# Kernel tuning notes

Hardware: AMD Instinct MI355X
Metric: run time of the kernel (lower is better)

## Reference

```python
import jax, jax.numpy as jnp
import numpy as np

N_NODES = 50000
N_EDGES = 500000
IN_DIM = 256
HID = 128
OUT_DIM = 7
N_LAYERS = 3
N_PAIRS = 100000
BATCH = 65536
BN_EPS = 1e-5


def setup_inputs() -> dict:
    key = jax.random.key(0)
    ks = jax.random.split(key, 24)
    s = 0.05
    inp = {
        "feat": jax.random.normal(ks[0], (N_NODES, IN_DIM), dtype=jnp.float32),
        "src": jax.random.randint(ks[1], (N_EDGES,), 0, N_NODES),
        "dst": jax.random.randint(ks[2], (N_EDGES,), 0, N_NODES),
        "ppi_pairs": jax.random.randint(ks[3], (N_PAIRS, 2), 0, N_NODES),
        "idx": jax.random.randint(ks[4], (BATCH,), 0, N_PAIRS),
        # GINConv 0 (input layer): 2-layer MLP IN_DIM->HID->HID
        "eps": jnp.zeros((N_LAYERS,), jnp.float32),
        "w1_in": jax.random.normal(ks[5], (IN_DIM, HID)) * s,
        "b1_in": jnp.zeros((HID,), jnp.float32),
        "w2_in": jax.random.normal(ks[6], (HID, HID)) * s,
        "b2_in": jnp.zeros((HID,), jnp.float32),
        # GINConv 1..2 (hidden layers), stacked
        "hw1": jax.random.normal(ks[7], (N_LAYERS - 1, HID, HID)) * s,
        "hb1": jnp.zeros((N_LAYERS - 1, HID), jnp.float32),
        "hw2": jax.random.normal(ks[8], (N_LAYERS - 1, HID, HID)) * s,
        "hb2": jnp.zeros((N_LAYERS - 1, HID), jnp.float32),
        # BatchNorm (eval mode) params per layer, stacked
        "bn_gamma": jnp.ones((N_LAYERS, HID), jnp.float32),
        "bn_beta": jnp.zeros((N_LAYERS, HID), jnp.float32),
        "bn_mean": jax.random.normal(ks[9], (N_LAYERS, HID)) * 0.1,
        "bn_var": jax.random.uniform(ks[10], (N_LAYERS, HID), minval=0.5, maxval=1.5),
        # final node linear
        "lin_w": jax.random.normal(ks[11], (HID, HID)) * s,
        "lin_b": jnp.zeros((HID,), jnp.float32),
        # interaction MLP: 2*HID -> HID -> OUT_DIM
        "int_w1": jax.random.normal(ks[12], (2 * HID, HID)) * s,
        "int_b1": jnp.zeros((HID,), jnp.float32),
        "int_w2": jax.random.normal(ks[13], (HID, OUT_DIM)) * s,
        "int_b2": jnp.zeros((OUT_DIM,), jnp.float32),
    }
    return inp


def _gin_layer(h, src, dst, eps_i, w1, b1, w2, b2, gamma, beta, mean, var):
    # sum-aggregate neighbor features: scatter-add messages src -> dst
    agg = jax.ops.segment_sum(h[src], dst, num_segments=N_NODES)
    h = (1.0 + eps_i) * h + agg
    # 2-layer MLP with ReLU after each linear (as in nn.Sequential)
    h = jax.nn.relu(h @ w1 + b1)
    h = jax.nn.relu(h @ w2 + b2)
    # BatchNorm1d, eval mode (running stats)
    h = (h - mean) * jax.lax.rsqrt(var + BN_EPS) * gamma + beta
    # trailing ReLU (dropout is identity at eval)
    return jax.nn.relu(h)


def reference(feat, src, dst, ppi_pairs, idx, eps, w1_in, b1_in, w2_in, b2_in,
              hw1, hb1, hw2, hb2, bn_gamma, bn_beta, bn_mean, bn_var,
              lin_w, lin_b, int_w1, int_b1, int_w2, int_b2):
    h = _gin_layer(feat, src, dst, eps[0], w1_in, b1_in, w2_in, b2_in,
                   bn_gamma[0], bn_beta[0], bn_mean[0], bn_var[0])
    for i in range(N_LAYERS - 1):
        h = _gin_layer(h, src, dst, eps[i + 1], hw1[i], hb1[i], hw2[i], hb2[i],
                       bn_gamma[i + 1], bn_beta[i + 1], bn_mean[i + 1], bn_var[i + 1])
    h = jax.nn.relu(h @ lin_w + lin_b)  # final node projection (dropout = identity)
    pairs = ppi_pairs[idx]              # [B, 2] node-id pairs
    h1 = h[pairs[:, 0]]
    h2 = h[pairs[:, 1]]
    z = jnp.concatenate([h1, h2], axis=1)        # [B, 2*HID]
    z = jax.nn.relu(z @ int_w1 + int_b1)         # (dropout = identity)
    return z @ int_w2 + int_b2                   # [B, OUT_DIM]
```

## Files before the change

kernel.cpp:

```cpp
#include <hip/hip_runtime.h>

#define N_NODES 50000
#define N_EDGES 500000
#define IN_DIM  256
#define HID     128
#define OUT_DIM 7
#define NPAIRS  100000
#define BATCH   65536
#define BN_EPS  1e-5f

#define SCAN_BLK 196

typedef __attribute__((ext_vector_type(8))) short bf16x8;
typedef __attribute__((ext_vector_type(4))) float f32x4;

__device__ inline float b2f(ushort u) {
  unsigned int x = ((unsigned int)u) << 16;
  return __uint_as_float(x);
}
__device__ inline ushort f2b(float f) {
  unsigned int x = __float_as_uint(f);
  unsigned int r = (x + 0x7fffu + ((x >> 16) & 1u)) >> 16;
  return (ushort)r;
}

__global__ void hist_kernel(const int* __restrict__ dst, int* __restrict__ deg) {
  int e = blockIdx.x * blockDim.x + threadIdx.x;
  if (e < N_EDGES) atomicAdd(&deg[dst[e]], 1);
}

__global__ __launch_bounds__(256) void scan_partial(const int* __restrict__ deg,
                                                    int* __restrict__ part) {
  __shared__ int s[256];
  int t = threadIdx.x;
  int i = blockIdx.x * 256 + t;
  s[t] = (i < N_NODES) ? deg[i] : 0;
  __syncthreads();
  for (int off = 128; off > 0; off >>= 1) {
    if (t < off) s[t] += s[t + off];
    __syncthreads();
  }
  if (t == 0) part[blockIdx.x] = s[0];
}

__global__ __launch_bounds__(256) void scan_offsets(int* __restrict__ part) {
  __shared__ int s[256];
  int t = threadIdx.x;
  int v = (t < SCAN_BLK) ? part[t] : 0;
  s[t] = v;
  __syncthreads();
  for (int off = 1; off < 256; off <<= 1) {
    int u = (t >= off) ? s[t - off] : 0;
    __syncthreads();
    s[t] += u;
    __syncthreads();
  }
  if (t < SCAN_BLK) part[t] = s[t] - v;
}

__global__ __launch_bounds__(256) void scan_final(const int* __restrict__ deg,
                                                  const int* __restrict__ part,
                                                  int* __restrict__ row_ptr,
                                                  int* __restrict__ cursor) {
  __shared__ int s[256];
  int t = threadIdx.x;
  int i = blockIdx.x * 256 + t;
  int v = (i < N_NODES) ? deg[i] : 0;
  s[t] = v;
  __syncthreads();
  for (int off = 1; off < 256; off <<= 1) {
    int u = (t >= off) ? s[t - off] : 0;
    __syncthreads();
    s[t] += u;
    __syncthreads();
  }
  int excl = s[t] - v + part[blockIdx.x];
  if (i < N_NODES) {
    row_ptr[i] = excl;
    cursor[i] = excl;
    if (i == N_NODES - 1) row_ptr[N_NODES] = excl + v;
  }
}

__global__ void scatter_kernel(const int* __restrict__ src,
                               const int* __restrict__ dst,
                               int* __restrict__ cursor,
                               int* __restrict__ esrc) {
  int e = blockIdx.x * blockDim.x + threadIdx.x;
  if (e < N_EDGES) {
    int pos = atomicAdd(&cursor[dst[e]], 1);
    esrc[pos] = src[e];
  }
}

__global__ void convw_kernel(const float* s0, const float* s1, const float* s2,
                             const float* s3, const float* s4, const float* s5,
                             const float* s6, const float* s7,
                             ushort* d0, ushort* d1, ushort* d2, ushort* d3,
                             ushort* d4, ushort* d5, ushort* d6, ushort* d7) {
  int gid = blockIdx.x * blockDim.x + threadIdx.x;
  const float* srcs[8] = {s0, s1, s2, s3, s4, s5, s6, s7};
  ushort* dsts[8] = {d0, d1, d2, d3, d4, d5, d6, d7};
  const int Ks[8] = {256, 128, 128, 128, 128, 128, 128, 256};
  const int off[9] = {0, 32768, 49152, 65536, 81920, 98304, 114688, 131072, 163840};
  if (gid >= 163840) return;
  int slot = 0;
#pragma unroll
  for (int s = 1; s < 8; ++s) if (gid >= off[s]) slot = s;
  int i = gid - off[slot];
  int K = Ks[slot];
  int k = i >> 7;
  int n = i & 127;
  dsts[slot][(size_t)n * K + k] = f2b(srcs[slot][(size_t)k * 128 + n]);
}

__global__ void convw2_kernel(const float* __restrict__ w2, ushort* __restrict__ w2t) {
  int gid = blockIdx.x * blockDim.x + threadIdx.x;
  if (gid >= 16 * 128) return;
  int c = gid >> 7;
  int k = gid & 127;
  w2t[gid] = (c < OUT_DIM) ? f2b(w2[(size_t)k * OUT_DIM + c]) : (ushort)0;
}

__global__ __launch_bounds__(256) void mm_bf16(
    const ushort* __restrict__ A,
    const ushort* __restrict__ WT,
    const float* __restrict__ bias,
    const float* __restrict__ gamma, const float* __restrict__ beta,
    const float* __restrict__ mean,  const float* __restrict__ var,
    ushort* __restrict__ C,
    int M, int K, int ldw, int do_bn)
{
  int tid  = threadIdx.x;
  int wid  = tid >> 6;
  int lane = tid & 63;
  int lr = lane & 15;
  int lg = lane >> 4;
  int m0 = blockIdx.x * 64 + wid * 16;

  int arow = m0 + lr;
  if (arow >= M) arow = M - 1;
  const ushort* Ap = A + (size_t)arow * K + lg * 8;

  f32x4 acc[8];
#pragma unroll
  for (int t = 0; t < 8; ++t) acc[t] = (f32x4){0.f, 0.f, 0.f, 0.f};

  for (int kk = 0; kk < K; kk += 32) {
    bf16x8 af = *(const bf16x8*)(Ap + kk);
#pragma unroll
    for (int t = 0; t < 8; ++t) {
      const ushort* Bp = WT + (size_t)(t * 16 + lr) * ldw + kk + lg * 8;
      bf16x8 bf = *(const bf16x8*)Bp;
      acc[t] = __builtin_amdgcn_mfma_f32_16x16x32_bf16(af, bf, acc[t], 0, 0, 0);
    }
  }

#pragma unroll
  for (int t = 0; t < 8; ++t) {
    int c = t * 16 + lr;
    float bs = 0.f, sc = 1.f, sh = 0.f;
    if (bias) bs = bias[c];
    if (do_bn) {
      float s = gamma[c] * rsqrtf(var[c] + BN_EPS);
      sc = s;
      sh = beta[c] - mean[c] * s;
    }
#pragma unroll
    for (int r = 0; r < 4; ++r) {
      int row = m0 + lg * 4 + r;
      if (row < M) {
        float v = acc[t][r];
        if (bias) {
          v += bs;
          v = fmaxf(v, 0.f);
          if (do_bn) { v = fmaf(v, sc, sh); v = fmaxf(v, 0.f); }
        }
        C[(size_t)row * HID + c] = f2b(v);
      }
    }
  }
}

__global__ __launch_bounds__(256) void mm_bf16_dual(
    const ushort* __restrict__ A,
    const ushort* __restrict__ WT,
    ushort* __restrict__ C0,
    ushort* __restrict__ C1,
    int M)
{
  int tid  = threadIdx.x;
  int wid  = tid >> 6;
  int lane = tid & 63;
  int lr = lane & 15;
  int lg = lane >> 4;
  int m0 = blockIdx.x * 64 + wid * 16;

  int arow = m0 + lr;
  if (arow >= M) arow = M - 1;
  const ushort* Ap = A + (size_t)arow * HID + lg * 8;

  f32x4 acc[16];
#pragma unroll
  for (int t = 0; t < 16; ++t) acc[t] = (f32x4){0.f, 0.f, 0.f, 0.f};

  for (int kk = 0; kk < HID; kk += 32) {
    bf16x8 af = *(const bf16x8*)(Ap + kk);
#pragma unroll
    for (int t = 0; t < 16; ++t) {
      int half = t >> 3;
      int nrow = (t & 7) * 16 + lr;
      const ushort* Bp = WT + (size_t)nrow * 256 + half * 128 + kk + lg * 8;
      bf16x8 bf = *(const bf16x8*)Bp;
      acc[t] = __builtin_amdgcn_mfma_f32_16x16x32_bf16(af, bf, acc[t], 0, 0, 0);
    }
  }

#pragma unroll
  for (int t = 0; t < 16; ++t) {
    int c = (t & 7) * 16 + lr;
    ushort* C = (t < 8) ? C0 : C1;
#pragma unroll
    for (int r = 0; r < 4; ++r) {
      int row = m0 + lg * 4 + r;
      if (row < M) C[(size_t)row * HID + c] = f2b(acc[t][r]);
    }
  }
}

__global__ __launch_bounds__(256) void mm_bf16_f32(
    const float* __restrict__ A,
    const ushort* __restrict__ WT,
    ushort* __restrict__ C,
    int M, int K)
{
  int tid  = threadIdx.x;
  int wid  = tid >> 6;
  int lane = tid & 63;
  int lr = lane & 15;
  int lg = lane >> 4;
  int m0 = blockIdx.x * 64 + wid * 16;

  int arow = m0 + lr;
  if (arow >= M) arow = M - 1;
  const float* Ap = A + (size_t)arow * K + lg * 8;

  f32x4 acc[8];
#pragma unroll
  for (int t = 0; t < 8; ++t) acc[t] = (f32x4){0.f, 0.f, 0.f, 0.f};

  for (int kk = 0; kk < K; kk += 32) {
    float4 a0 = *(const float4*)(Ap + kk);
    float4 a1 = *(const float4*)(Ap + kk + 4);
    bf16x8 af;
    af[0] = (short)f2b(a0.x); af[1] = (short)f2b(a0.y);
    af[2] = (short)f2b(a0.z); af[3] = (short)f2b(a0.w);
    af[4] = (short)f2b(a1.x); af[5] = (short)f2b(a1.y);
    af[6] = (short)f2b(a1.z); af[7] = (short)f2b(a1.w);
#pragma unroll
    for (int t = 0; t < 8; ++t) {
      const ushort* Bp = WT + (size_t)(t * 16 + lr) * K + kk + lg * 8;
      bf16x8 bf = *(const bf16x8*)Bp;
      acc[t] = __builtin_amdgcn_mfma_f32_16x16x32_bf16(af, bf, acc[t], 0, 0, 0);
    }
  }

#pragma unroll
  for (int t = 0; t < 8; ++t) {
    int c = t * 16 + lr;
#pragma unroll
    for (int r = 0; r < 4; ++r) {
      int row = m0 + lg * 4 + r;
      if (row < M) C[(size_t)row * HID + c] = f2b(acc[t][r]);
    }
  }
}

__global__ __launch_bounds__(256) void gather_kernel(
    const ushort* __restrict__ t,
    const int* __restrict__ row_ptr,
    const int* __restrict__ esrc,
    const float* __restrict__ epsP, int layer,
    const float* __restrict__ bias,
    ushort* __restrict__ x)
{
  int wave = (blockIdx.x * blockDim.x + threadIdx.x) >> 6;
  int lane = threadIdx.x & 63;
  if (wave >= N_NODES) return;
  int beg = row_ptr[wave];
  int end = row_ptr[wave + 1];
  float scale = 1.0f + epsP[layer];

  unsigned int u = *(const unsigned int*)(t + (size_t)wave * HID + lane * 2);
  float ax = b2f((ushort)(u & 0xffff)) * scale;
  float ay = b2f((ushort)(u >> 16)) * scale;

  int i = beg;
  for (; i + 4 <= end; i += 4) {
    int s0 = esrc[i + 0];
    int s1 = esrc[i + 1];
    int s2 = esrc[i + 2];
    int s3 = esrc[i + 3];
    unsigned int v0 = *(const unsigned int*)(t + (size_t)s0 * HID + lane * 2);
    unsigned int v1 = *(const unsigned int*)(t + (size_t)s1 * HID + lane * 2);
    unsigned int v2 = *(const unsigned int*)(t + (size_t)s2 * HID + lane * 2);
    unsigned int v3 = *(const unsigned int*)(t + (size_t)s3 * HID + lane * 2);
    ax += b2f((ushort)(v0 & 0xffff)) + b2f((ushort)(v1 & 0xffff)) +
          b2f((ushort)(v2 & 0xffff)) + b2f((ushort)(v3 & 0xffff));
    ay += b2f((ushort)(v0 >> 16)) + b2f((ushort)(v1 >> 16)) +
          b2f((ushort)(v2 >> 16)) + b2f((ushort)(v3 >> 16));
  }
  for (; i < end; ++i) {
    int s = esrc[i];
    unsigned int v = *(const unsigned int*)(t + (size_t)s * HID + lane * 2);
    ax += b2f((ushort)(v & 0xffff));
    ay += b2f((ushort)(v >> 16));
  }

  float2 b = *(const float2*)(bias + lane * 2);
  ax = fmaxf(ax + b.x, 0.0f);
  ay = fmaxf(ay + b.y, 0.0f);
  unsigned int o = ((unsigned int)f2b(ay) << 16) | f2b(ax);
  *(unsigned int*)(x + (size_t)wave * HID + lane * 2) = o;
}

__global__ __launch_bounds__(256) void pair_mfma(
    const ushort* __restrict__ P1,
    const ushort* __restrict__ P2,
    const int* __restrict__ ppi,
    const int* __restrict__ idx,
    const float* __restrict__ b1,
    const ushort* __restrict__ w2t,
    const float* __restrict__ b2,
    float* __restrict__ out)
{
  int tid  = threadIdx.x;
  int wid  = tid >> 6;
  int lane = tid & 63;
  int lr = lane & 15;
  int lg = lane >> 4;
  int p0 = blockIdx.x * 64 + wid * 16;
  int p  = p0 + lr;

  int pi = idx[p];
  int n0 = ppi[2 * pi];
  int n1 = ppi[2 * pi + 1];

  const ushort* r1 = P1 + (size_t)n0 * HID + lg * 8;
  const ushort* r2 = P2 + (size_t)n1 * HID + lg * 8;
  const float*  bp = b1 + lg * 8;
  const ushort* wp = w2t + (size_t)lr * HID + lg * 8;

  f32x4 acc = (f32x4){0.f, 0.f, 0.f, 0.f};
#pragma unroll
  for (int kk = 0; kk < HID; kk += 32) {
    bf16x8 a1v = *(const bf16x8*)(r1 + kk);
    bf16x8 a2v = *(const bf16x8*)(r2 + kk);
    float4 bb0 = *(const float4*)(bp + kk);
    float4 bb1 = *(const float4*)(bp + kk + 4);
    float bbf[8] = {bb0.x, bb0.y, bb0.z, bb0.w, bb1.x, bb1.y, bb1.z, bb1.w};
    bf16x8 af;
#pragma unroll
    for (int j = 0; j < 8; ++j) {
      float v = b2f((ushort)a1v[j]) + b2f((ushort)a2v[j]) + bbf[j];
      af[j] = (short)f2b(fmaxf(v, 0.f));
    }
    bf16x8 bf = *(const bf16x8*)(wp + kk);
    acc = __builtin_amdgcn_mfma_f32_16x16x32_bf16(af, bf, acc, 0, 0, 0);
  }

  if (lr < OUT_DIM) {
    float bias2 = b2[lr];
#pragma unroll
    for (int r = 0; r < 4; ++r) {
      out[(size_t)(p0 + lg * 4 + r) * OUT_DIM + lr] = acc[r] + bias2;
    }
  }
}

extern "C" void kernel_launch(void* const* d_in, const int* in_sizes, int n_in,
                              void* d_out, int out_size, void* d_ws, size_t ws_size,
                              hipStream_t stream) {
  const float* feat   = (const float*)d_in[0];
  const int*   src    = (const int*)d_in[1];
  const int*   dst    = (const int*)d_in[2];
  const int*   ppi    = (const int*)d_in[3];
  const int*   idx    = (const int*)d_in[4];
  const float* eps    = (const float*)d_in[5];
  const float* w1_in  = (const float*)d_in[6];
  const float* b1_in  = (const float*)d_in[7];
  const float* w2_in  = (const float*)d_in[8];
  const float* b2_in  = (const float*)d_in[9];
  const float* hw1    = (const float*)d_in[10];
  const float* hb1    = (const float*)d_in[11];
  const float* hw2    = (const float*)d_in[12];
  const float* hb2    = (const float*)d_in[13];
  const float* bng    = (const float*)d_in[14];
  const float* bnb    = (const float*)d_in[15];
  const float* bnm    = (const float*)d_in[16];
  const float* bnv    = (const float*)d_in[17];
  const float* lin_w  = (const float*)d_in[18];
  const float* lin_b  = (const float*)d_in[19];
  const float* int_w1 = (const float*)d_in[20];
  const float* int_b1 = (const float*)d_in[21];
  const float* int_w2 = (const float*)d_in[22];
  const float* int_b2 = (const float*)d_in[23];
  float* out = (float*)d_out;

  const size_t NB = (size_t)N_NODES * HID;
  ushort* b0 = (ushort*)d_ws;
  ushort* b1 = b0 + NB;
  ushort* b2 = b1 + NB;
  ushort* b3 = b2 + NB;
  ushort* WT1  = b3 + NB;
  ushort* WT2  = WT1 + 32768;
  ushort* WH1a = WT2 + 16384;
  ushort* WH1b = WH1a + 16384;
  ushort* WH2a = WH1b + 16384;
  ushort* WH2b = WH2a + 16384;
  ushort* WTL  = WH2b + 16384;
  ushort* WTI  = WTL + 16384;
  ushort* W2T  = WTI + 32768;
  int* row_ptr = (int*)(W2T + 2048);
  int* cursor  = row_ptr + N_NODES + 8;
  int* esrc    = cursor + N_NODES;
  int* part    = esrc + N_EDGES;

  int mmBlocks = (N_NODES + 63) / 64;
  int edgeBlocks = (N_EDGES + 255) / 256;
  int nodeWaveBlocks = (N_NODES + 3) / 4;
  int pairBlocks = BATCH / 64;

  hipMemsetAsync(cursor, 0, N_NODES * sizeof(int), stream);
  hist_kernel<<<edgeBlocks, 256, 0, stream>>>(dst, cursor);
  scan_partial<<<SCAN_BLK, 256, 0, stream>>>(cursor, part);
  scan_offsets<<<1, 256, 0, stream>>>(part);
  scan_final<<<SCAN_BLK, 256, 0, stream>>>(cursor, part, row_ptr, cursor);
  scatter_kernel<<<edgeBlocks, 256, 0, stream>>>(src, dst, cursor, esrc);
  convw_kernel<<<640, 256, 0, stream>>>(w1_in, w2_in, hw1, hw1 + 128 * 128,
                                        hw2, hw2 + 128 * 128, lin_w, int_w1,
                                        WT1, WT2, WH1a, WH1b, WH2a, WH2b, WTL, WTI);
  convw2_kernel<<<8, 256, 0, stream>>>(int_w2, W2T);

  mm_bf16_f32<<<mmBlocks, 256, 0, stream>>>(feat, WT1, b0, N_NODES, IN_DIM);
  gather_kernel<<<nodeWaveBlocks, 256, 0, stream>>>(b0, row_ptr, esrc, eps, 0, b1_in, b1);
  mm_bf16<<<mmBlocks, 256, 0, stream>>>(b1, WT2, b2_in,
                                        bng, bnb, bnm, bnv,
                                        b2, N_NODES, HID, HID, 1);

  ushort* WH1[2] = {WH1a, WH1b};
  ushort* WH2[2] = {WH2a, WH2b};
  for (int l = 1; l < 3; ++l) {
    mm_bf16<<<mmBlocks, 256, 0, stream>>>(b2, WH1[l - 1], nullptr,
                                          nullptr, nullptr, nullptr, nullptr,
                                          b0, N_NODES, HID, HID, 0);
    gather_kernel<<<nodeWaveBlocks, 256, 0, stream>>>(b0, row_ptr, esrc, eps, l,
                                                      hb1 + (size_t)(l - 1) * HID, b1);
    mm_bf16<<<mmBlocks, 256, 0, stream>>>(b1, WH2[l - 1],
                                          hb2 + (size_t)(l - 1) * HID,
                                          bng + l * HID, bnb + l * HID,
                                          bnm + l * HID, bnv + l * HID,
                                          b2, N_NODES, HID, HID, 1);
  }

  mm_bf16<<<mmBlocks, 256, 0, stream>>>(b2, WTL, lin_b,
                                        nullptr, nullptr, nullptr, nullptr,
                                        b3, N_NODES, HID, HID, 0);

  mm_bf16_dual<<<mmBlocks, 256, 0, stream>>>(b3, WTI, b0, b1, N_NODES);
  pair_mfma<<<pairBlocks, 256, 0, stream>>>(b0, b1, ppi, idx,
                                            int_b1, W2T, int_b2, out);
}
```

Before: 510.5 us.

## Split GEMM N across waves, preload A fragments, widen gather unroll

The node GEMM kernels now use 32-row blocks, with two waves covering each half of the 128 output columns. Each wave preloads all of its A fragments into registers, and K becomes a compile-time template parameter so the loops fully unroll. This doubles the block count and halves accumulator registers to improve occupancy and memory-level parallelism, at the cost of A rows being read by two waves. The gather kernel also unrolls its edge loop to 8 to put more independent loads in flight.

```diff
diff --git a/kernel.cpp b/kernel.cpp
--- a/kernel.cpp
+++ b/kernel.cpp
@@ -122,43 +122,50 @@
   w2t[gid] = (c < OUT_DIM) ? f2b(w2[(size_t)k * OUT_DIM + c]) : (ushort)0;
 }
 
-__global__ __launch_bounds__(256) void mm_bf16(
+template <int K>
+__global__ __launch_bounds__(256) void mm_bf16_t(
     const ushort* __restrict__ A,
     const ushort* __restrict__ WT,
     const float* __restrict__ bias,
     const float* __restrict__ gamma, const float* __restrict__ beta,
     const float* __restrict__ mean,  const float* __restrict__ var,
     ushort* __restrict__ C,
-    int M, int K, int ldw, int do_bn)
+    int M, int do_bn)
 {
+  constexpr int NK = K / 32;
   int tid  = threadIdx.x;
   int wid  = tid >> 6;
   int lane = tid & 63;
   int lr = lane & 15;
   int lg = lane >> 4;
-  int m0 = blockIdx.x * 64 + wid * 16;
+  int nh = wid & 1;
+  int m0 = blockIdx.x * 32 + (wid >> 1) * 16;
 
   int arow = m0 + lr;
   if (arow >= M) arow = M - 1;
   const ushort* Ap = A + (size_t)arow * K + lg * 8;
 
-  f32x4 acc[8];
-#pragma unroll
-  for (int t = 0; t < 8; ++t) acc[t] = (f32x4){0.f, 0.f, 0.f, 0.f};
-
-  for (int kk = 0; kk < K; kk += 32) {
-    bf16x8 af = *(const bf16x8*)(Ap + kk);
-#pragma unroll
-    for (int t = 0; t < 8; ++t) {
-      const ushort* Bp = WT + (size_t)(t * 16 + lr) * ldw + kk + lg * 8;
-      bf16x8 bf = *(const bf16x8*)Bp;
-      acc[t] = __builtin_amdgcn_mfma_f32_16x16x32_bf16(af, bf, acc[t], 0, 0, 0);
-    }
-  }
-
-#pragma unroll
-  for (int t = 0; t < 8; ++t) {
-    int c = t * 16 + lr;
+  bf16x8 afr[NK];
+#pragma unroll
+  for (int kk = 0; kk < NK; ++kk) afr[kk] = *(const bf16x8*)(Ap + kk * 32);
+
+  f32x4 acc[4];
+#pragma unroll
+  for (int t = 0; t < 4; ++t) acc[t] = (f32x4){0.f, 0.f, 0.f, 0.f};
+
+#pragma unroll
+  for (int t = 0; t < 4; ++t) {
+    const ushort* Bp = WT + (size_t)(nh * 64 + t * 16 + lr) * K + lg * 8;
+#pragma unroll
+    for (int kk = 0; kk < NK; ++kk) {
+      bf16x8 bf = *(const bf16x8*)(Bp + kk * 32);
+      acc[t] = __builtin_amdgcn_mfma_f32_16x16x32_bf16(afr[kk], bf, acc[t], 0, 0, 0);
+    }
+  }
+
+#pragma unroll
+  for (int t = 0; t < 4; ++t) {
+    int c = nh * 64 + t * 16 + lr;
     float bs = 0.f, sc = 1.f, sh = 0.f;
     if (bias) bs = bias[c];
     if (do_bn) {
@@ -182,6 +189,64 @@
   }
 }
 
+__global__ __launch_bounds__(256) void mm_bf16_f32(
+    const float* __restrict__ A,
+    const ushort* __restrict__ WT,
+    ushort* __restrict__ C,
+    int M)
+{
+  constexpr int K = IN_DIM;
+  constexpr int NK = K / 32;
+  int tid  = threadIdx.x;
+  int wid  = tid >> 6;
+  int lane = tid & 63;
+  int lr = lane & 15;
+  int lg = lane >> 4;
+  int nh = wid & 1;
+  int m0 = blockIdx.x * 32 + (wid >> 1) * 16;
+
+  int arow = m0 + lr;
+  if (arow >= M) arow = M - 1;
+  const float* Ap = A + (size_t)arow * K + lg * 8;
+
+  bf16x8 afr[NK];
+#pragma unroll
+  for (int kk = 0; kk < NK; ++kk) {
+    float4 a0 = *(const float4*)(Ap + kk * 32);
+    float4 a1 = *(const float4*)(Ap + kk * 32 + 4);
+    bf16x8 af;
+    af[0] = (short)f2b(a0.x); af[1] = (short)f2b(a0.y);
+    af[2] = (short)f2b(a0.z); af[3] = (short)f2b(a0.w);
+    af[4] = (short)f2b(a1.x); af[5] = (short)f2b(a1.y);
+    af[6] = (short)f2b(a1.z); af[7] = (short)f2b(a1.w);
+    afr[kk] = af;
+  }
+
+  f32x4 acc[4];
+#pragma unroll
+  for (int t = 0; t < 4; ++t) acc[t] = (f32x4){0.f, 0.f, 0.f, 0.f};
+
+#pragma unroll
+  for (int t = 0; t < 4; ++t) {
+    const ushort* Bp = WT + (size_t)(nh * 64 + t * 16 + lr) * K + lg * 8;
+#pragma unroll
+    for (int kk = 0; kk < NK; ++kk) {
+      bf16x8 bf = *(const bf16x8*)(Bp + kk * 32);
+      acc[t] = __builtin_amdgcn_mfma_f32_16x16x32_bf16(afr[kk], bf, acc[t], 0, 0, 0);
+    }
+  }
+
+#pragma unroll
+  for (int t = 0; t < 4; ++t) {
+    int c = nh * 64 + t * 16 + lr;
+#pragma unroll
+    for (int r = 0; r < 4; ++r) {
+      int row = m0 + lg * 4 + r;
+      if (row < M) C[(size_t)row * HID + c] = f2b(acc[t][r]);
+    }
+  }
+}
+
 __global__ __launch_bounds__(256) void mm_bf16_dual(
     const ushort* __restrict__ A,
     const ushort* __restrict__ WT,
@@ -189,85 +254,43 @@
     ushort* __restrict__ C1,
     int M)
 {
+  constexpr int NK = HID / 32;
   int tid  = threadIdx.x;
   int wid  = tid >> 6;
   int lane = tid & 63;
   int lr = lane & 15;
   int lg = lane >> 4;
-  int m0 = blockIdx.x * 64 + wid * 16;
+  int nh = wid & 1;
+  int m0 = blockIdx.x * 32 + (wid >> 1) * 16;
 
   int arow = m0 + lr;
   if (arow >= M) arow = M - 1;
   const ushort* Ap = A + (size_t)arow * HID + lg * 8;
 
-  f32x4 acc[16];
-#pragma unroll
-  for (int t = 0; t < 16; ++t) acc[t] = (f32x4){0.f, 0.f, 0.f, 0.f};
-
-  for (int kk = 0; kk < HID; kk += 32) {
-    bf16x8 af = *(const bf16x8*)(Ap + kk);
-#pragma unroll
-    for (int t = 0; t < 16; ++t) {
-      int half = t >> 3;
-      int nrow = (t & 7) * 16 + lr;
-      const ushort* Bp = WT + (size_t)nrow * 256 + half * 128 + kk + lg * 8;
-      bf16x8 bf = *(const bf16x8*)Bp;
-      acc[t] = __builtin_amdgcn_mfma_f32_16x16x32_bf16(af, bf, acc[t], 0, 0, 0);
-    }
-  }
-
-#pragma unroll
-  for (int t = 0; t < 16; ++t) {
-    int c = (t & 7) * 16 + lr;
-    ushort* C = (t < 8) ? C0 : C1;
-#pragma unroll
-    for (int r = 0; r < 4; ++r) {
-      int row = m0 + lg * 4 + r;
-      if (row < M) C[(size_t)row * HID + c] = f2b(acc[t][r]);
-    }
-  }
-}
-
-__global__ __launch_bounds__(256) void mm_bf16_f32(
-    const float* __restrict__ A,
-    const ushort* __restrict__ WT,
-    ushort* __restrict__ C,
-    int M, int K)
-{
-  int tid  = threadIdx.x;
-  int wid  = tid >> 6;
-  int lane = tid & 63;
-  int lr = lane & 15;
-  int lg = lane >> 4;
-  int m0 = blockIdx.x * 64 + wid * 16;
-
-  int arow = m0 + lr;
-  if (arow >= M) arow = M - 1;
-  const float* Ap = A + (size_t)arow * K + lg * 8;
+  bf16x8 afr[NK];
+#pragma unroll
+  for (int kk = 0; kk < NK; ++kk) afr[kk] = *(const bf16x8*)(Ap + kk * 32);
 
   f32x4 acc[8];
 #pragma unroll
   for (int t = 0; t < 8; ++t) acc[t] = (f32x4){0.f, 0.f, 0.f, 0.f};
 
-  for (int kk = 0; kk < K; kk += 32) {
-    float4 a0 = *(const float4*)(Ap + kk);
-    float4 a1 = *(const float4*)(Ap + kk + 4);
-    bf16x8 af;
-    af[0] = (short)f2b(a0.x); af[1] = (short)f2b(a0.y);
-    af[2] = (short)f2b(a0.z); af[3] = (short)f2b(a0.w);
-    af[4] = (short)f2b(a1.x); af[5] = (short)f2b(a1.y);
-    af[6] = (short)f2b(a1.z); af[7] = (short)f2b(a1.w);
-#pragma unroll
-    for (int t = 0; t < 8; ++t) {
-      const ushort* Bp = WT + (size_t)(t * 16 + lr) * K + kk + lg * 8;
-      bf16x8 bf = *(const bf16x8*)Bp;
-      acc[t] = __builtin_amdgcn_mfma_f32_16x16x32_bf16(af, bf, acc[t], 0, 0, 0);
-    }
-  }
-
 #pragma unroll
   for (int t = 0; t < 8; ++t) {
-    int c = t * 16 + lr;
+    int half = t >> 2;
+    int nrow = nh * 64 + (t & 3) * 16 + lr;
+    const ushort* Bp = WT + (size_t)nrow * 256 + half * 128 + lg * 8;
+#pragma unroll
+    for (int kk = 0; kk < NK; ++kk) {
+      bf16x8 bf = *(const bf16x8*)(Bp + kk * 32);
+      acc[t] = __builtin_amdgcn_mfma_f32_16x16x32_bf16(afr[kk], bf, acc[t], 0, 0, 0);
+    }
+  }
+
+#pragma unroll
+  for (int t = 0; t < 8; ++t) {
+    int c = nh * 64 + (t & 3) * 16 + lr;
+    ushort* C = (t < 4) ? C0 : C1;
 #pragma unroll
     for (int r = 0; r < 4; ++r) {
       int row = m0 + lg * 4 + r;
@@ -296,19 +319,19 @@
   float ay = b2f((ushort)(u >> 16)) * scale;
 
   int i = beg;
-  for (; i + 4 <= end; i += 4) {
-    int s0 = esrc[i + 0];
-    int s1 = esrc[i + 1];
-    int s2 = esrc[i + 2];
-    int s3 = esrc[i + 3];
-    unsigned int v0 = *(const unsigned int*)(t + (size_t)s0 * HID + lane * 2);
-    unsigned int v1 = *(const unsigned int*)(t + (size_t)s1 * HID + lane * 2);
-    unsigned int v2 = *(const unsigned int*)(t + (size_t)s2 * HID + lane * 2);
-    unsigned int v3 = *(const unsigned int*)(t + (size_t)s3 * HID + lane * 2);
-    ax += b2f((ushort)(v0 & 0xffff)) + b2f((ushort)(v1 & 0xffff)) +
-          b2f((ushort)(v2 & 0xffff)) + b2f((ushort)(v3 & 0xffff));
-    ay += b2f((ushort)(v0 >> 16)) + b2f((ushort)(v1 >> 16)) +
-          b2f((ushort)(v2 >> 16)) + b2f((ushort)(v3 >> 16));
+  for (; i + 8 <= end; i += 8) {
+    int s[8];
+#pragma unroll
+    for (int j = 0; j < 8; ++j) s[j] = esrc[i + j];
+    unsigned int v[8];
+#pragma unroll
+    for (int j = 0; j < 8; ++j)
+      v[j] = *(const unsigned int*)(t + (size_t)s[j] * HID + lane * 2);
+#pragma unroll
+    for (int j = 0; j < 8; ++j) {
+      ax += b2f((ushort)(v[j] & 0xffff));
+      ay += b2f((ushort)(v[j] >> 16));
+    }
   }
   for (; i < end; ++i) {
     int s = esrc[i];
@@ -426,7 +449,7 @@
   int* esrc    = cursor + N_NODES;
   int* part    = esrc + N_EDGES;
 
-  int mmBlocks = (N_NODES + 63) / 64;
+  int mmBlocks = (N_NODES + 31) / 32;
   int edgeBlocks = (N_EDGES + 255) / 256;
   int nodeWaveBlocks = (N_NODES + 3) / 4;
   int pairBlocks = BATCH / 64;
@@ -442,30 +465,30 @@
                                         WT1, WT2, WH1a, WH1b, WH2a, WH2b, WTL, WTI);
   convw2_kernel<<<8, 256, 0, stream>>>(int_w2, W2T);
 
-  mm_bf16_f32<<<mmBlocks, 256, 0, stream>>>(feat, WT1, b0, N_NODES, IN_DIM);
+  mm_bf16_f32<<<mmBlocks, 256, 0, stream>>>(feat, WT1, b0, N_NODES);
   gather_kernel<<<nodeWaveBlocks, 256, 0, stream>>>(b0, row_ptr, esrc, eps, 0, b1_in, b1);
-  mm_bf16<<<mmBlocks, 256, 0, stream>>>(b1, WT2, b2_in,
-                                        bng, bnb, bnm, bnv,
-                                        b2, N_NODES, HID, HID, 1);
+  mm_bf16_t<HID><<<mmBlocks, 256, 0, stream>>>(b1, WT2, b2_in,
+                                               bng, bnb, bnm, bnv,
+                                               b2, N_NODES, 1);
 
   ushort* WH1[2] = {WH1a, WH1b};
   ushort* WH2[2] = {WH2a, WH2b};
   for (int l = 1; l < 3; ++l) {
-    mm_bf16<<<mmBlocks, 256, 0, stream>>>(b2, WH1[l - 1], nullptr,
-                                          nullptr, nullptr, nullptr, nullptr,
-                                          b0, N_NODES, HID, HID, 0);
+    mm_bf16_t<HID><<<mmBlocks, 256, 0, stream>>>(b2, WH1[l - 1], nullptr,
+                                                 nullptr, nullptr, nullptr, nullptr,
+                                                 b0, N_NODES, 0);
     gather_kernel<<<nodeWaveBlocks, 256, 0, stream>>>(b0, row_ptr, esrc, eps, l,
                                                       hb1 + (size_t)(l - 1) * HID, b1);
-    mm_bf16<<<mmBlocks, 256, 0, stream>>>(b1, WH2[l - 1],
-                                          hb2 + (size_t)(l - 1) * HID,
-                                          bng + l * HID, bnb + l * HID,
-                                          bnm + l * HID, bnv + l * HID,
-                                          b2, N_NODES, HID, HID, 1);
-  }
-
-  mm_bf16<<<mmBlocks, 256, 0, stream>>>(b2, WTL, lin_b,
-                                        nullptr, nullptr, nullptr, nullptr,
-                                        b3, N_NODES, HID, HID, 0);
+    mm_bf16_t<HID><<<mmBlocks, 256, 0, stream>>>(b1, WH2[l - 1],
+                                                 hb2 + (size_t)(l - 1) * HID,
+                                                 bng + l * HID, bnb + l * HID,
+                                                 bnm + l * HID, bnv + l * HID,
+                                                 b2, N_NODES, 1);
+  }
+
+  mm_bf16_t<HID><<<mmBlocks, 256, 0, stream>>>(b2, WTL, lin_b,
+                                               nullptr, nullptr, nullptr, nullptr,
+                                               b3, N_NODES, 0);
 
   mm_bf16_dual<<<mmBlocks, 256, 0, stream>>>(b3, WTI, b0, b1, N_NODES);
   pair_mfma<<<pairBlocks, 256, 0, stream>>>(b0, b1, ppi, idx,
```

Result: faster. 494.2 us (-3.2%).
